# Optimization experiments

Measured on AMD Instinct MI355X. Metric: run time of the kernel, lower is better.

## Reference

```python
import jax, jax.numpy as jnp
import numpy as np

NS, NT = 4000, 4096
E_S, E_T = 64000, 65536
D_IN, D_H, N_LAYERS = 128, 256, 3
SINK_ITERS = 10
EPS = 1e-10
ALPHA = 20.0


def scatter_mean(vals, idx, n):
    # torch_geometric aggr='mean': sum then divide by count (0 where count==0)
    s = jax.ops.segment_sum(vals, idx, num_segments=n)
    c = jax.ops.segment_sum(jnp.ones((idx.shape[0],), vals.dtype), idx, num_segments=n)
    return s / jnp.maximum(c, 1.0)[:, None]


def rel_cnn(x, edge_index, layers, final_w, final_b):
    # RelCNN(batch_norm=False, cat=True, lin=True), eval mode (dropout off)
    src, dst = edge_index[0], edge_index[1]
    n = x.shape[0]
    xs = [x]
    h = x
    for (w1, w2, wr, br) in layers:
        out1 = scatter_mean((h @ w1)[src], dst, n)  # source->target mean agg
        out2 = scatter_mean((h @ w2)[dst], src, n)  # target->source mean agg
        h = jax.nn.relu(h @ wr + br + out1 + out2)  # RelConv: root + out1 + out2
        xs.append(h)
    return jnp.concatenate(xs, axis=-1) @ final_w + final_b


def sinkhorn(S):
    # Sinkhorn(max_iter=10, eps=1e-10) with dummy_row=True, exp=True, alpha=20
    ns, nt = S.shape  # ns <= nt: pad dummy rows set to eps
    pad = jnp.full((nt - ns, nt), EPS, S.dtype)
    s = jnp.concatenate([S, pad], axis=0) + EPS
    s = jnp.exp(ALPHA * s)
    for i in range(SINK_ITERS):
        if i % 2 == 1:  # row normalization
            s = s / s.sum(axis=1, keepdims=True)
        else:           # column normalization
            s = s / s.sum(axis=0, keepdims=True)
    return s[:ns, :]  # drop dummy rows


def l2norm(x):
    return x / jnp.maximum(jnp.linalg.norm(x, axis=1, keepdims=True), 1e-12)


def setup_inputs() -> dict:
    key = jax.random.key(0)
    ks = jax.random.split(key, 20)
    d = {
        'x_s': jax.random.normal(ks[0], (NS, D_IN), jnp.float32),
        'x_t': jax.random.normal(ks[1], (NT, D_IN), jnp.float32),
        'edges': jax.random.randint(ks[2], (2, E_S), 0, NS, jnp.int32),
        'edget': jax.random.randint(ks[3], (2, E_T), 0, NT, jnp.int32),
    }
    k = 4
    fan = D_IN
    for l in range(N_LAYERS):
        sc = 1.0 / np.sqrt(fan)
        d[f'W1_{l}'] = jax.random.normal(ks[k], (fan, D_H), jnp.float32) * sc; k += 1
        d[f'W2_{l}'] = jax.random.normal(ks[k], (fan, D_H), jnp.float32) * sc; k += 1
        d[f'Wr_{l}'] = jax.random.normal(ks[k], (fan, D_H), jnp.float32) * sc; k += 1
        d[f'br_{l}'] = jax.random.normal(ks[k], (D_H,), jnp.float32) * 0.01; k += 1
        fan = D_H
    fin = D_IN + N_LAYERS * D_H
    d['final_w'] = jax.random.normal(ks[k], (fin, D_H), jnp.float32) * (0.01 / np.sqrt(fin)); k += 1
    d['final_b'] = jax.random.normal(ks[k], (D_H,), jnp.float32) * 0.001
    return d


def reference(x_s, x_t, edges, edget,
              W1_0, W2_0, Wr_0, br_0,
              W1_1, W2_1, Wr_1, br_1,
              W1_2, W2_2, Wr_2, br_2,
              final_w, final_b):
    layers = [(W1_0, W2_0, Wr_0, br_0), (W1_1, W2_1, Wr_1, br_1), (W1_2, W2_2, Wr_2, br_2)]
    h_s = rel_cnn(x_s, edges, layers, final_w, final_b)   # [NS, D_H]
    h_t = rel_cnn(x_t, edget, layers, final_w, final_b)   # [NT, D_H]
    match = l2norm(h_s) @ l2norm(h_t).T                   # [NS, NT]
    return sinkhorn(match)
```

## Files before the change

### kernel.cpp

```cpp
#include <hip/hip_runtime.h>
#include <hip/hip_bf16.h>

#define NS_N 4000
#define NT_N 4096
#define NTOT 8096
#define ES_E 64000
#define ET_E 65536
#define ETOT 129536
#define D_IN 128
#define D_H 256
#define CAT_D 896
#define TMP_D 768
#define NDUM (NT_N - NS_N)
#define ALPHA_F 20.0f
#define EPS_F 1e-10f

typedef __attribute__((ext_vector_type(8))) short bf16x8;
typedef __attribute__((ext_vector_type(4))) float f32x4;

__device__ inline short f2bf(float v) {
    __hip_bfloat16 b = __float2bfloat16(v);
    return *reinterpret_cast<short*>(&b);
}
__device__ inline float bf2f(short s) {
    __hip_bfloat16 b = *reinterpret_cast<__hip_bfloat16*>(&s);
    return __bfloat162float(b);
}
__device__ inline void splitf(float v, short& hi, short& lo) {
    hi = f2bf(v);
    lo = f2bf(v - bf2f(hi));
}

typedef __attribute__((address_space(1))) const char gas_t;
typedef __attribute__((address_space(3))) char las_t;
__device__ inline void gload16(const short* g, short* l) {
    __builtin_amdgcn_global_load_lds((gas_t*)g, (las_t*)l, 16, 0, 0);
}

template<int EPI, bool COLSUM>
__global__ __launch_bounds__(256) void mfma_gemm_kernel(
    const short* __restrict__ Ahi, const short* __restrict__ Alo,
    const short* __restrict__ Bhi, const short* __restrict__ Blo,
    const float* __restrict__ bias, float* __restrict__ C,
    float* __restrict__ colacc,
    int M, int N, int K, int lda, int ldb, int ldc)
{
    __shared__ __align__(16) short sAh[2][4096];
    __shared__ __align__(16) short sAl[2][4096];
    __shared__ __align__(16) short sBh[2][4096];
    __shared__ __align__(16) short sBl[2][4096];
    const int bm = blockIdx.x * 128;
    const int bn = blockIdx.y * 128;
    const int tid = threadIdx.x;
    const int lane = tid & 63, wv = tid >> 6;
    const int wr = wv >> 1, wc = wv & 1;
    const int lr = lane & 15, lg = lane >> 4;
    const int srow = lane >> 2, sseg = (lane & 3) * 8;

    f32x4 acc[4][4];
    #pragma unroll
    for (int i = 0; i < 4; ++i)
        #pragma unroll
        for (int j = 0; j < 4; ++j) {
            f32x4 z = {0.f, 0.f, 0.f, 0.f};
            acc[i][j] = z;
        }

    auto stage = [&](int buf, int k0) {
        const short* src; short* dst; int rowbase, ld, maxrow;
        if (wv == 0)      { src = Ahi; dst = &sAh[buf][0]; rowbase = bm; ld = lda; maxrow = M - 1; }
        else if (wv == 1) { src = Alo; dst = &sAl[buf][0]; rowbase = bm; ld = lda; maxrow = M - 1; }
        else if (wv == 2) { src = Bhi; dst = &sBh[buf][0]; rowbase = bn; ld = ldb; maxrow = N - 1; }
        else              { src = Blo; dst = &sBl[buf][0]; rowbase = bn; ld = ldb; maxrow = N - 1; }
        #pragma unroll
        for (int q = 0; q < 8; ++q) {
            int gr = min(rowbase + q * 16 + srow, maxrow);
            gload16(src + (size_t)gr * ld + k0 + sseg, dst + q * 512);
        }
    };

    stage(0, 0);
    __syncthreads();
    int cur = 0;
    const int NTILES = K >> 5;
    for (int t0 = 0; t0 < NTILES; ++t0) {
        if (t0 + 1 < NTILES) stage(cur ^ 1, (t0 + 1) << 5);
        bf16x8 ah[4], al[4], bh[4], bl[4];
        #pragma unroll
        for (int i = 0; i < 4; ++i) {
            int oa = (wr * 64 + i * 16 + lr) * 32 + lg * 8;
            ah[i] = *reinterpret_cast<const bf16x8*>(&sAh[cur][oa]);
            al[i] = *reinterpret_cast<const bf16x8*>(&sAl[cur][oa]);
            int ob = (wc * 64 + i * 16 + lr) * 32 + lg * 8;
            bh[i] = *reinterpret_cast<const bf16x8*>(&sBh[cur][ob]);
            bl[i] = *reinterpret_cast<const bf16x8*>(&sBl[cur][ob]);
        }
        #pragma unroll
        for (int i = 0; i < 4; ++i)
            #pragma unroll
            for (int j = 0; j < 4; ++j) {
                acc[i][j] = __builtin_amdgcn_mfma_f32_16x16x32_bf16(ah[i], bh[j], acc[i][j], 0, 0, 0);
                acc[i][j] = __builtin_amdgcn_mfma_f32_16x16x32_bf16(ah[i], bl[j], acc[i][j], 0, 0, 0);
                acc[i][j] = __builtin_amdgcn_mfma_f32_16x16x32_bf16(al[i], bh[j], acc[i][j], 0, 0, 0);
            }
        __syncthreads();
        cur ^= 1;
    }

    float colp[4] = {0.f, 0.f, 0.f, 0.f};
    #pragma unroll
    for (int i = 0; i < 4; ++i) {
        #pragma unroll
        for (int j = 0; j < 4; ++j) {
            int col = bn + wc * 64 + j * 16 + lr;
            #pragma unroll
            for (int rr = 0; rr < 4; ++rr) {
                int row = bm + wr * 64 + i * 16 + lg * 4 + rr;
                if (row < M) {
                    float v = acc[i][j][rr];
                    if (EPI == 1) v += bias[col];
                    if (EPI == 2) v = expf(ALPHA_F * (v + EPS_F));
                    C[(size_t)row * ldc + col] = v;
                    if (COLSUM) colp[j] += v;
                }
            }
        }
    }
    if (COLSUM) {
        #pragma unroll
        for (int j = 0; j < 4; ++j) {
            float v = colp[j];
            v += __shfl_xor(v, 16);
            v += __shfl_xor(v, 32);
            if (lg == 0) atomicAdd(&colacc[bn + wc * 64 + j * 16 + lr], v);
        }
    }
}

__global__ __launch_bounds__(256) void prep_kernel(
    const float* __restrict__ xs, const float* __restrict__ xt,
    const float* __restrict__ W1a, const float* __restrict__ W2a, const float* __restrict__ Wra,
    const float* __restrict__ W1b, const float* __restrict__ W2b, const float* __restrict__ Wrb,
    const float* __restrict__ W1c, const float* __restrict__ W2c, const float* __restrict__ Wrc,
    const float* __restrict__ WF,
    short* __restrict__ WThi0, short* __restrict__ WTlo0,
    short* __restrict__ WThi1, short* __restrict__ WTlo1,
    short* __restrict__ WThi2, short* __restrict__ WTlo2,
    short* __restrict__ WFhi, short* __restrict__ WFlo,
    short* __restrict__ CAThi, short* __restrict__ CATlo,
    int* __restrict__ zbase)
{
    int blk = blockIdx.x;
    const int t = threadIdx.x;
    if (blk < 80) {
        int idx = blk * 256 + t;
        if (idx < NT_N + 2 * NTOT) zbase[idx] = 0;
        return;
    }
    blk -= 80;
    if (blk < 384 + 768 + 768) {
        const float *W1, *W2, *Wr; short *WThi, *WTlo; int K, idx;
        if (blk < 384)      { W1 = W1a; W2 = W2a; Wr = Wra; WThi = WThi0; WTlo = WTlo0; K = 128; idx = blk * 256 + t; }
        else if (blk < 1152){ W1 = W1b; W2 = W2b; Wr = Wrb; WThi = WThi1; WTlo = WTlo1; K = 256; idx = (blk - 384) * 256 + t; }
        else                { W1 = W1c; W2 = W2c; Wr = Wrc; WThi = WThi2; WTlo = WTlo2; K = 256; idx = (blk - 1152) * 256 + t; }
        int k = idx / TMP_D, c = idx % TMP_D;
        float v = (c < 256) ? W1[k * 256 + c]
                : (c < 512) ? W2[k * 256 + (c - 256)]
                            : Wr[k * 256 + (c - 512)];
        short hi, lo;
        splitf(v, hi, lo);
        WThi[(size_t)c * K + k] = hi;
        WTlo[(size_t)c * K + k] = lo;
        return;
    }
    blk -= 1920;
    if (blk < 896) {
        int idx = blk * 256 + t;
        int k = idx / D_H, n = idx % D_H;
        short hi, lo;
        splitf(WF[idx], hi, lo);
        WFhi[(size_t)n * CAT_D + k] = hi;
        WFlo[(size_t)n * CAT_D + k] = lo;
        return;
    }
    blk -= 896;
    {
        int idx = blk * 256 + t;
        int i = idx >> 7, d = idx & 127;
        float v = (i < NS_N) ? xs[(size_t)i * D_IN + d] : xt[(size_t)(i - NS_N) * D_IN + d];
        short hi, lo;
        splitf(v, hi, lo);
        CAThi[(size_t)i * CAT_D + d] = hi;
        CATlo[(size_t)i * CAT_D + d] = lo;
    }
}

__global__ void count2_kernel(const int* __restrict__ es, const int* __restrict__ et,
                              int* __restrict__ cin, int* __restrict__ cout)
{
    int e = blockIdx.x * 256 + threadIdx.x;
    int dir = blockIdx.y;
    int* cnt = dir ? cout : cin;
    if (e < ES_E) {
        int key = dir ? es[e] : es[e + ES_E];
        atomicAdd(&cnt[key], 1);
    } else if (e < ETOT) {
        int e2 = e - ES_E;
        int key = dir ? et[e2] : et[e2 + ET_E];
        atomicAdd(&cnt[key + NS_N], 1);
    }
}

__global__ __launch_bounds__(256) void scan2_kernel(const int* __restrict__ cin,
                                                    const int* __restrict__ cout,
                                                    int* __restrict__ rpin, int* __restrict__ rpout,
                                                    int* __restrict__ curin, int* __restrict__ curout)
{
    const int* cnt = blockIdx.x ? cout : cin;
    int* rowptr = blockIdx.x ? rpout : rpin;
    int* cur = blockIdx.x ? curout : curin;
    __shared__ int sums[256];
    const int t = threadIdx.x;
    const int per = (NTOT + 255) / 256;
    const int lo = t * per, hi = min((t + 1) * per, NTOT);
    int s = 0;
    for (int i = lo; i < hi; ++i) s += cnt[i];
    sums[t] = s;
    __syncthreads();
    for (int off = 1; off < 256; off <<= 1) {
        int v = (t >= off) ? sums[t - off] : 0;
        __syncthreads();
        sums[t] += v;
        __syncthreads();
    }
    int base = (t == 0) ? 0 : sums[t - 1];
    for (int i = lo; i < hi; ++i) { rowptr[i] = base; cur[i] = base; base += cnt[i]; }
    if (t == 255) rowptr[NTOT] = base;
}

__global__ void fill2_kernel(const int* __restrict__ es, const int* __restrict__ et,
                             int* __restrict__ curin, int* __restrict__ curout,
                             int* __restrict__ ciin, int* __restrict__ ciout)
{
    int e = blockIdx.x * 256 + threadIdx.x;
    int dir = blockIdx.y;
    int* cur = dir ? curout : curin;
    int* ci = dir ? ciout : ciin;
    int key, val, off;
    if (e < ES_E) {
        key = dir ? es[e] : es[e + ES_E];
        val = dir ? es[e + ES_E] : es[e];
        off = 0;
    } else if (e < ETOT) {
        int e2 = e - ES_E;
        key = dir ? et[e2] : et[e2 + ET_E];
        val = dir ? et[e2 + ET_E] : et[e2];
        off = NS_N;
    } else return;
    int pos = atomicAdd(&cur[key + off], 1);
    ci[pos] = val + off;
}

__global__ __launch_bounds__(256) void gather_combine_kernel(
    const float* __restrict__ TMP,
    const int* __restrict__ rp_in, const int* __restrict__ ci_in,
    const int* __restrict__ rp_out, const int* __restrict__ ci_out,
    const float* __restrict__ br, short* __restrict__ CAThi, short* __restrict__ CATlo,
    int catoff)
{
    int node = blockIdx.x * 4 + (threadIdx.x >> 6);
    if (node >= NTOT) return;
    int d = (threadIdx.x & 63) * 4;

    float4 a1 = make_float4(0.f, 0.f, 0.f, 0.f);
    int b0 = rp_in[node], e0 = rp_in[node + 1];
    for (int e = b0; e < e0; ++e) {
        const float4 v = *reinterpret_cast<const float4*>(&TMP[(size_t)ci_in[e] * TMP_D + d]);
        a1.x += v.x; a1.y += v.y; a1.z += v.z; a1.w += v.w;
    }
    float s1 = 1.f / (float)max(e0 - b0, 1);

    float4 a2 = make_float4(0.f, 0.f, 0.f, 0.f);
    int b1 = rp_out[node], e1 = rp_out[node + 1];
    for (int e = b1; e < e1; ++e) {
        const float4 v = *reinterpret_cast<const float4*>(&TMP[(size_t)ci_out[e] * TMP_D + 256 + d]);
        a2.x += v.x; a2.y += v.y; a2.z += v.z; a2.w += v.w;
    }
    float s2 = 1.f / (float)max(e1 - b1, 1);

    const float4 rt = *reinterpret_cast<const float4*>(&TMP[(size_t)node * TMP_D + 512 + d]);
    const float4 bb = *reinterpret_cast<const float4*>(&br[d]);
    float o[4];
    o[0] = fmaxf(rt.x + bb.x + a1.x * s1 + a2.x * s2, 0.f);
    o[1] = fmaxf(rt.y + bb.y + a1.y * s1 + a2.y * s2, 0.f);
    o[2] = fmaxf(rt.z + bb.z + a1.z * s1 + a2.z * s2, 0.f);
    o[3] = fmaxf(rt.w + bb.w + a1.w * s1 + a2.w * s2, 0.f);
    short h[4], l[4];
    #pragma unroll
    for (int q = 0; q < 4; ++q) splitf(o[q], h[q], l[q]);
    *reinterpret_cast<short4*>(&CAThi[(size_t)node * CAT_D + catoff + d]) = make_short4(h[0], h[1], h[2], h[3]);
    *reinterpret_cast<short4*>(&CATlo[(size_t)node * CAT_D + catoff + d]) = make_short4(l[0], l[1], l[2], l[3]);
}

__global__ __launch_bounds__(256) void l2norm_kernel(const float* __restrict__ in,
                                                     short* __restrict__ outhi,
                                                     short* __restrict__ outlo, int N)
{
    int row = blockIdx.x * 4 + (threadIdx.x >> 6);
    if (row >= N) return;
    int d = (threadIdx.x & 63) * 4;
    float4 v = *reinterpret_cast<const float4*>(&in[(size_t)row * D_H + d]);
    float s = v.x * v.x + v.y * v.y + v.z * v.z + v.w * v.w;
    #pragma unroll
    for (int off = 32; off; off >>= 1) s += __shfl_xor(s, off);
    float inv = 1.f / fmaxf(sqrtf(s), 1e-12f);
    float o[4] = {v.x * inv, v.y * inv, v.z * inv, v.w * inv};
    short h[4], l[4];
    #pragma unroll
    for (int q = 0; q < 4; ++q) splitf(o[q], h[q], l[q]);
    *reinterpret_cast<short4*>(&outhi[(size_t)row * D_H + d]) = make_short4(h[0], h[1], h[2], h[3]);
    *reinterpret_cast<short4*>(&outlo[(size_t)row * D_H + d]) = make_short4(l[0], l[1], l[2], l[3]);
}

__global__ __launch_bounds__(256) void colsum_kernel(
    const float* __restrict__ s0, const float* __restrict__ r, float* __restrict__ tsum)
{
    int j4 = blockIdx.x * 256 + threadIdx.x;
    int i0 = blockIdx.y * 32;
    int iend = min(i0 + 32, NS_N);
    float4 s = make_float4(0.f, 0.f, 0.f, 0.f);
    for (int i = i0; i < iend; ++i) {
        float ri = r[i];
        const float4 v = *reinterpret_cast<const float4*>(&s0[(size_t)i * NT_N + j4 * 4]);
        s.x += ri * v.x; s.y += ri * v.y; s.z += ri * v.z; s.w += ri * v.w;
    }
    atomicAdd(&tsum[j4 * 4 + 0], s.x);
    atomicAdd(&tsum[j4 * 4 + 1], s.y);
    atomicAdd(&tsum[j4 * 4 + 2], s.z);
    atomicAdd(&tsum[j4 * 4 + 3], s.w);
}

template<bool FIRST, bool FUSE_OUT>
__global__ __launch_bounds__(256) void rowsum_kernel(
    const float* __restrict__ s0, const float* __restrict__ tsum,
    const float* __restrict__ rdR, float* __restrict__ rdW,
    float* __restrict__ r, float* __restrict__ tsumNext,
    float* __restrict__ out, float dummyv)
{
    int i = blockIdx.x;
    int t = threadIdx.x;
    if (i < 16) tsumNext[i * 256 + t] = 0.f;
    float rdv = FIRST ? 1.f : rdR[0];
    float dd = (float)NDUM * dummyv * rdv;
    float s = 0.f;
    if (i < NS_N) {
        for (int j4 = t; j4 < NT_N / 4; j4 += 256) {
            const float4 v = *reinterpret_cast<const float4*>(&s0[(size_t)i * NT_N + j4 * 4]);
            const float4 ts = *reinterpret_cast<const float4*>(&tsum[j4 * 4]);
            s += v.x / (ts.x + dd) + v.y / (ts.y + dd) + v.z / (ts.z + dd) + v.w / (ts.w + dd);
        }
    } else {
        for (int j = t; j < NT_N; j += 256) s += 1.f / (tsum[j] + dd);
    }
    #pragma unroll
    for (int off = 32; off; off >>= 1) s += __shfl_xor(s, off);
    __shared__ float ws[4];
    __shared__ float ri_sh;
    if ((t & 63) == 0) ws[t >> 6] = s;
    __syncthreads();
    if (t == 0) {
        float tot = ws[0] + ws[1] + ws[2] + ws[3];
        if (i < NS_N) { r[i] = 1.f / tot; ri_sh = 1.f / tot; }
        else rdW[0] = 1.f / (dummyv * tot);
    }
    if (FUSE_OUT) {
        __syncthreads();
        if (i < NS_N) {
            float ri = ri_sh;
            for (int j4 = t; j4 < NT_N / 4; j4 += 256) {
                const float4 v = *reinterpret_cast<const float4*>(&s0[(size_t)i * NT_N + j4 * 4]);
                const float4 ts = *reinterpret_cast<const float4*>(&tsum[j4 * 4]);
                float4 o = make_float4(ri * v.x / (ts.x + dd), ri * v.y / (ts.y + dd),
                                       ri * v.z / (ts.z + dd), ri * v.w / (ts.w + dd));
                *reinterpret_cast<float4*>(&out[(size_t)i * NT_N + j4 * 4]) = o;
            }
        }
    }
}

extern "C" void kernel_launch(void* const* d_in, const int* in_sizes, int n_in,
                              void* d_out, int out_size, void* d_ws, size_t ws_size,
                              hipStream_t stream)
{
    const float* x_s = (const float*)d_in[0];
    const float* x_t = (const float*)d_in[1];
    const int* edges = (const int*)d_in[2];
    const int* edget = (const int*)d_in[3];
    const float* W1[3] = {(const float*)d_in[4], (const float*)d_in[8], (const float*)d_in[12]};
    const float* W2[3] = {(const float*)d_in[5], (const float*)d_in[9], (const float*)d_in[13]};
    const float* Wr[3] = {(const float*)d_in[6], (const float*)d_in[10], (const float*)d_in[14]};
    const float* br[3] = {(const float*)d_in[7], (const float*)d_in[11], (const float*)d_in[15]};
    const float* final_w = (const float*)d_in[16];
    const float* final_b = (const float*)d_in[17];
    float* out = (float*)d_out;

    float* W = (float*)d_ws;
    size_t off = 0;
    float* S0 = W + off;  off += (size_t)NS_N * NT_N;
    float* TMP = W + off; off += (size_t)NTOT * TMP_D;
    short* CAThi = (short*)(W + off); off += (size_t)NTOT * CAT_D / 2;
    short* CATlo = (short*)(W + off); off += (size_t)NTOT * CAT_D / 2;
    const int fan[3] = {D_IN, D_H, D_H};
    short* WThi[3]; short* WTlo[3];
    for (int l = 0; l < 3; ++l) {
        WThi[l] = (short*)(W + off); off += (size_t)TMP_D * fan[l] / 2;
        WTlo[l] = (short*)(W + off); off += (size_t)TMP_D * fan[l] / 2;
    }
    short* WFhi = (short*)(W + off); off += (size_t)D_H * CAT_D / 2;
    short* WFlo = (short*)(W + off); off += (size_t)D_H * CAT_D / 2;
    float* RVEC = W + off; off += NS_N;
    float* RD   = W + off; off += 8;
    float* TSA  = W + off; off += NT_N;
    int* CNT_IN  = (int*)(W + off); off += NTOT;
    int* CNT_OUT = (int*)(W + off); off += NTOT;
    float* TSB  = W + off; off += NT_N;
    int* RP_IN   = (int*)(W + off); off += NTOT + 1;
    int* RP_OUT  = (int*)(W + off); off += NTOT + 3;
    int* CUR_IN  = (int*)(W + off); off += NTOT;
    int* CUR_OUT = (int*)(W + off); off += NTOT;
    int* CI_IN   = (int*)(W + off); off += ETOT;
    int* CI_OUT  = (int*)(W + off); off += ETOT;
    float* HFIN = TMP;
    short* HNhi = (short*)(TMP + (size_t)NTOT * D_H);
    short* HNlo = (short*)(TMP + (size_t)NTOT * D_H + (size_t)NTOT * D_H / 2);

    const int cat_off[4] = {0, 128, 384, 640};

    prep_kernel<<<6944, 256, 0, stream>>>(
        x_s, x_t,
        W1[0], W2[0], Wr[0], W1[1], W2[1], Wr[1], W1[2], W2[2], Wr[2], final_w,
        WThi[0], WTlo[0], WThi[1], WTlo[1], WThi[2], WTlo[2], WFhi, WFlo,
        CAThi, CATlo, (int*)TSA);

    {
        dim3 gc((ETOT + 255) / 256, 2);
        count2_kernel<<<gc, 256, 0, stream>>>(edges, edget, CNT_IN, CNT_OUT);
        scan2_kernel<<<2, 256, 0, stream>>>(CNT_IN, CNT_OUT, RP_IN, RP_OUT, CUR_IN, CUR_OUT);
        fill2_kernel<<<gc, 256, 0, stream>>>(edges, edget, CUR_IN, CUR_OUT, CI_IN, CI_OUT);
    }

    for (int l = 0; l < 3; ++l) {
        dim3 gg((NTOT + 127) / 128, TMP_D / 128);
        mfma_gemm_kernel<0, false><<<gg, 256, 0, stream>>>(
            CAThi + cat_off[l], CATlo + cat_off[l], WThi[l], WTlo[l], nullptr, TMP, nullptr,
            NTOT, TMP_D, fan[l], CAT_D, fan[l], TMP_D);
        gather_combine_kernel<<<(NTOT + 3) / 4, 256, 0, stream>>>(
            TMP, RP_IN, CI_IN, RP_OUT, CI_OUT, br[l], CAThi, CATlo, cat_off[l + 1]);
    }

    {
        dim3 gf((NTOT + 127) / 128, D_H / 128);
        mfma_gemm_kernel<1, false><<<gf, 256, 0, stream>>>(
            CAThi, CATlo, WFhi, WFlo, final_b, HFIN, nullptr,
            NTOT, D_H, CAT_D, CAT_D, CAT_D, D_H);
        l2norm_kernel<<<(NTOT + 3) / 4, 256, 0, stream>>>(HFIN, HNhi, HNlo, NTOT);
    }

    {
        dim3 gm((NS_N + 127) / 128, NT_N / 128);
        mfma_gemm_kernel<2, true><<<gm, 256, 0, stream>>>(
            HNhi, HNlo, HNhi + (size_t)NS_N * D_H, HNlo + (size_t)NS_N * D_H, nullptr, S0, TSA,
            NS_N, NT_N, D_H, D_H, D_H, NT_N);
    }

    const float dummyv = expf(ALPHA_F * (EPS_F + EPS_F));
    dim3 gcs(NT_N / 1024, (NS_N + 31) / 32);
    rowsum_kernel<true, false><<<NS_N + 1, 256, 0, stream>>>(
        S0, TSA, nullptr, &RD[0], RVEC, TSB, nullptr, dummyv);
    colsum_kernel<<<gcs, 256, 0, stream>>>(S0, RVEC, TSB);
    rowsum_kernel<false, false><<<NS_N + 1, 256, 0, stream>>>(
        S0, TSB, &RD[0], &RD[1], RVEC, TSA, nullptr, dummyv);
    colsum_kernel<<<gcs, 256, 0, stream>>>(S0, RVEC, TSA);
    rowsum_kernel<false, false><<<NS_N + 1, 256, 0, stream>>>(
        S0, TSA, &RD[1], &RD[0], RVEC, TSB, nullptr, dummyv);
    colsum_kernel<<<gcs, 256, 0, stream>>>(S0, RVEC, TSB);
    rowsum_kernel<false, false><<<NS_N + 1, 256, 0, stream>>>(
        S0, TSB, &RD[0], &RD[1], RVEC, TSA, nullptr, dummyv);
    colsum_kernel<<<gcs, 256, 0, stream>>>(S0, RVEC, TSA);
    rowsum_kernel<false, true><<<NS_N + 1, 256, 0, stream>>>(
        S0, TSA, &RD[1], &RD[0], RVEC, TSB, out, dummyv);
}
```

Baseline: 580.4 us.

## Fuse Sinkhorn row/col passes, swizzle GEMM LDS, vectorize epilogue, smaller final tile

Each Sinkhorn row-normalize and column-sum pair becomes one kernel. A block of 8 rows computes the row sums against cached reciprocal column sums in LDS, then accumulates the scaled rows into the next column sums with atomics, using three rotating buffers. This halves the number of passes over the 4000x4096 S matrix. The GEMM gains an XOR-style LDS swizzle to reduce bank conflicts, swapped MFMA operands so the epilogue writes float4 rows and does float4 colsum atomics, and a BM=64 tile for the final projection to raise block count.

After: 802.7 us. 38.3% more time.

```diff
diff --git a/kernel.cpp b/kernel.cpp
--- a/kernel.cpp
+++ b/kernel.cpp
@@ -37,7 +37,7 @@
     __builtin_amdgcn_global_load_lds((gas_t*)g, (las_t*)l, 16, 0, 0);
 }
 
-template<int EPI, bool COLSUM>
+template<int BM, int EPI, bool COLSUM>
 __global__ __launch_bounds__(256) void mfma_gemm_kernel(
     const short* __restrict__ Ahi, const short* __restrict__ Alo,
     const short* __restrict__ Bhi, const short* __restrict__ Blo,
@@ -45,21 +45,22 @@
     float* __restrict__ colacc,
     int M, int N, int K, int lda, int ldb, int ldc)
 {
-    __shared__ __align__(16) short sAh[2][4096];
-    __shared__ __align__(16) short sAl[2][4096];
+    constexpr int MI = BM / 32;
+    constexpr int WH = BM / 2;
+    __shared__ __align__(16) short sAh[2][BM * 32];
+    __shared__ __align__(16) short sAl[2][BM * 32];
     __shared__ __align__(16) short sBh[2][4096];
     __shared__ __align__(16) short sBl[2][4096];
-    const int bm = blockIdx.x * 128;
+    const int bm = blockIdx.x * BM;
     const int bn = blockIdx.y * 128;
     const int tid = threadIdx.x;
     const int lane = tid & 63, wv = tid >> 6;
     const int wr = wv >> 1, wc = wv & 1;
     const int lr = lane & 15, lg = lane >> 4;
-    const int srow = lane >> 2, sseg = (lane & 3) * 8;
-
-    f32x4 acc[4][4];
+
+    f32x4 acc[MI][4];
     #pragma unroll
-    for (int i = 0; i < 4; ++i)
+    for (int i = 0; i < MI; ++i)
         #pragma unroll
         for (int j = 0; j < 4; ++j) {
             f32x4 z = {0.f, 0.f, 0.f, 0.f};
@@ -72,12 +73,17 @@
         else if (wv == 1) { src = Alo; dst = &sAl[buf][0]; rowbase = bm; ld = lda; maxrow = M - 1; }
         else if (wv == 2) { src = Bhi; dst = &sBh[buf][0]; rowbase = bn; ld = ldb; maxrow = N - 1; }
         else              { src = Blo; dst = &sBl[buf][0]; rowbase = bn; ld = ldb; maxrow = N - 1; }
+        const int nq = (wv < 2) ? (BM / 16) : 8;
         #pragma unroll
         for (int q = 0; q < 8; ++q) {
-            int gr = min(rowbase + q * 16 + srow, maxrow);
-            gload16(src + (size_t)gr * ld + k0 + sseg, dst + q * 512);
+            if (q >= nq) break;
+            int row = q * 16 + (lane >> 2);
+            int seg = ((lane & 3) - (row >> 1)) & 3;
+            int gr = min(rowbase + row, maxrow);
+            gload16(src + (size_t)gr * ld + k0 + seg * 8, dst + (q * 64 + lane) * 8);
         }
     };
+    auto ldsoff = [](int row, int g) { return (row * 4 + ((g + (row >> 1)) & 3)) * 8; };
 
     stage(0, 0);
     __syncthreads();
@@ -85,43 +91,57 @@
     const int NTILES = K >> 5;
     for (int t0 = 0; t0 < NTILES; ++t0) {
         if (t0 + 1 < NTILES) stage(cur ^ 1, (t0 + 1) << 5);
-        bf16x8 ah[4], al[4], bh[4], bl[4];
-        #pragma unroll
-        for (int i = 0; i < 4; ++i) {
-            int oa = (wr * 64 + i * 16 + lr) * 32 + lg * 8;
+        bf16x8 ah[MI], al[MI], bh[4], bl[4];
+        #pragma unroll
+        for (int i = 0; i < MI; ++i) {
+            int oa = ldsoff(wr * WH + i * 16 + lr, lg);
             ah[i] = *reinterpret_cast<const bf16x8*>(&sAh[cur][oa]);
             al[i] = *reinterpret_cast<const bf16x8*>(&sAl[cur][oa]);
-            int ob = (wc * 64 + i * 16 + lr) * 32 + lg * 8;
-            bh[i] = *reinterpret_cast<const bf16x8*>(&sBh[cur][ob]);
-            bl[i] = *reinterpret_cast<const bf16x8*>(&sBl[cur][ob]);
-        }
-        #pragma unroll
-        for (int i = 0; i < 4; ++i)
+        }
+        #pragma unroll
+        for (int j = 0; j < 4; ++j) {
+            int ob = ldsoff(wc * 64 + j * 16 + lr, lg);
+            bh[j] = *reinterpret_cast<const bf16x8*>(&sBh[cur][ob]);
+            bl[j] = *reinterpret_cast<const bf16x8*>(&sBl[cur][ob]);
+        }
+        #pragma unroll
+        for (int i = 0; i < MI; ++i)
             #pragma unroll
             for (int j = 0; j < 4; ++j) {
-                acc[i][j] = __builtin_amdgcn_mfma_f32_16x16x32_bf16(ah[i], bh[j], acc[i][j], 0, 0, 0);
-                acc[i][j] = __builtin_amdgcn_mfma_f32_16x16x32_bf16(ah[i], bl[j], acc[i][j], 0, 0, 0);
-                acc[i][j] = __builtin_amdgcn_mfma_f32_16x16x32_bf16(al[i], bh[j], acc[i][j], 0, 0, 0);
+                acc[i][j] = __builtin_amdgcn_mfma_f32_16x16x32_bf16(bh[j], ah[i], acc[i][j], 0, 0, 0);
+                acc[i][j] = __builtin_amdgcn_mfma_f32_16x16x32_bf16(bl[j], ah[i], acc[i][j], 0, 0, 0);
+                acc[i][j] = __builtin_amdgcn_mfma_f32_16x16x32_bf16(bh[j], al[i], acc[i][j], 0, 0, 0);
             }
         __syncthreads();
         cur ^= 1;
     }
 
-    float colp[4] = {0.f, 0.f, 0.f, 0.f};
+    float4 csum[4];
+    if (COLSUM) {
+        #pragma unroll
+        for (int j = 0; j < 4; ++j) csum[j] = make_float4(0.f, 0.f, 0.f, 0.f);
+    }
     #pragma unroll
-    for (int i = 0; i < 4; ++i) {
-        #pragma unroll
-        for (int j = 0; j < 4; ++j) {
-            int col = bn + wc * 64 + j * 16 + lr;
+    for (int i = 0; i < MI; ++i) {
+        int row = bm + wr * WH + i * 16 + lr;
+        if (row < M) {
             #pragma unroll
-            for (int rr = 0; rr < 4; ++rr) {
-                int row = bm + wr * 64 + i * 16 + lg * 4 + rr;
-                if (row < M) {
-                    float v = acc[i][j][rr];
-                    if (EPI == 1) v += bias[col];
-                    if (EPI == 2) v = expf(ALPHA_F * (v + EPS_F));
-                    C[(size_t)row * ldc + col] = v;
-                    if (COLSUM) colp[j] += v;
+            for (int j = 0; j < 4; ++j) {
+                int col = bn + wc * 64 + j * 16 + lg * 4;
+                float4 v = make_float4(acc[i][j][0], acc[i][j][1], acc[i][j][2], acc[i][j][3]);
+                if (EPI == 1) {
+                    const float4 bb = *reinterpret_cast<const float4*>(&bias[col]);
+                    v.x += bb.x; v.y += bb.y; v.z += bb.z; v.w += bb.w;
+                }
+                if (EPI == 2) {
+                    v.x = expf(ALPHA_F * (v.x + EPS_F));
+                    v.y = expf(ALPHA_F * (v.y + EPS_F));
+                    v.z = expf(ALPHA_F * (v.z + EPS_F));
+                    v.w = expf(ALPHA_F * (v.w + EPS_F));
+                }
+                *reinterpret_cast<float4*>(&C[(size_t)row * ldc + col]) = v;
+                if (COLSUM) {
+                    csum[j].x += v.x; csum[j].y += v.y; csum[j].z += v.z; csum[j].w += v.w;
                 }
             }
         }
@@ -129,14 +149,24 @@
     if (COLSUM) {
         #pragma unroll
         for (int j = 0; j < 4; ++j) {
-            float v = colp[j];
-            v += __shfl_xor(v, 16);
-            v += __shfl_xor(v, 32);
-            if (lg == 0) atomicAdd(&colacc[bn + wc * 64 + j * 16 + lr], v);
-        }
-    }
-}
-
+            float4 t = csum[j];
+            #pragma unroll
+            for (int m = 1; m < 16; m <<= 1) {
+                t.x += __shfl_xor(t.x, m); t.y += __shfl_xor(t.y, m);
+                t.z += __shfl_xor(t.z, m); t.w += __shfl_xor(t.w, m);
+            }
+            if (lr == 0) {
+                int col = bn + wc * 64 + j * 16 + lg * 4;
+                atomicAdd(&colacc[col + 0], t.x);
+                atomicAdd(&colacc[col + 1], t.y);
+                atomicAdd(&colacc[col + 2], t.z);
+                atomicAdd(&colacc[col + 3], t.w);
+            }
+        }
+    }
+}
+
+#define ZERO_N (NT_N + 2 * NTOT + NT_N)
 __global__ __launch_bounds__(256) void prep_kernel(
     const float* __restrict__ xs, const float* __restrict__ xt,
     const float* __restrict__ W1a, const float* __restrict__ W2a, const float* __restrict__ Wra,
@@ -152,12 +182,12 @@
 {
     int blk = blockIdx.x;
     const int t = threadIdx.x;
-    if (blk < 80) {
+    if (blk < 96) {
         int idx = blk * 256 + t;
-        if (idx < NT_N + 2 * NTOT) zbase[idx] = 0;
+        if (idx < ZERO_N) zbase[idx] = 0;
         return;
     }
-    blk -= 80;
+    blk -= 96;
     if (blk < 384 + 768 + 768) {
         const float *W1, *W2, *Wr; short *WThi, *WTlo; int K, idx;
         if (blk < 384)      { W1 = W1a; W2 = W2a; Wr = Wra; WThi = WThi0; WTlo = WTlo0; K = 128; idx = blk * 256 + t; }
@@ -322,68 +352,95 @@
     *reinterpret_cast<short4*>(&outlo[(size_t)row * D_H + d]) = make_short4(l[0], l[1], l[2], l[3]);
 }
 
-__global__ __launch_bounds__(256) void colsum_kernel(
-    const float* __restrict__ s0, const float* __restrict__ r, float* __restrict__ tsum)
-{
-    int j4 = blockIdx.x * 256 + threadIdx.x;
-    int i0 = blockIdx.y * 32;
-    int iend = min(i0 + 32, NS_N);
-    float4 s = make_float4(0.f, 0.f, 0.f, 0.f);
-    for (int i = i0; i < iend; ++i) {
-        float ri = r[i];
-        const float4 v = *reinterpret_cast<const float4*>(&s0[(size_t)i * NT_N + j4 * 4]);
-        s.x += ri * v.x; s.y += ri * v.y; s.z += ri * v.z; s.w += ri * v.w;
-    }
-    atomicAdd(&tsum[j4 * 4 + 0], s.x);
-    atomicAdd(&tsum[j4 * 4 + 1], s.y);
-    atomicAdd(&tsum[j4 * 4 + 2], s.z);
-    atomicAdd(&tsum[j4 * 4 + 3], s.w);
-}
-
-template<bool FIRST, bool FUSE_OUT>
-__global__ __launch_bounds__(256) void rowsum_kernel(
+template<bool FIRST, bool OUT>
+__global__ __launch_bounds__(256) void sinkfuse_kernel(
     const float* __restrict__ s0, const float* __restrict__ tsum,
     const float* __restrict__ rdR, float* __restrict__ rdW,
-    float* __restrict__ r, float* __restrict__ tsumNext,
+    float* __restrict__ tsnext, float* __restrict__ tszero,
     float* __restrict__ out, float dummyv)
 {
-    int i = blockIdx.x;
-    int t = threadIdx.x;
-    if (i < 16) tsumNext[i * 256 + t] = 0.f;
-    float rdv = FIRST ? 1.f : rdR[0];
-    float dd = (float)NDUM * dummyv * rdv;
-    float s = 0.f;
-    if (i < NS_N) {
-        for (int j4 = t; j4 < NT_N / 4; j4 += 256) {
-            const float4 v = *reinterpret_cast<const float4*>(&s0[(size_t)i * NT_N + j4 * 4]);
-            const float4 ts = *reinterpret_cast<const float4*>(&tsum[j4 * 4]);
-            s += v.x / (ts.x + dd) + v.y / (ts.y + dd) + v.z / (ts.z + dd) + v.w / (ts.w + dd);
-        }
-    } else {
-        for (int j = t; j < NT_N; j += 256) s += 1.f / (tsum[j] + dd);
-    }
+    const int bid = blockIdx.x;
+    const int t = threadIdx.x;
+    if (!OUT && bid >= 501) {
+        tszero[(bid - 501) * 256 + t] = 0.f;
+        return;
+    }
+    __shared__ float4 cl[1024];
+    __shared__ float wsred[4];
+    const float dd = (float)NDUM * dummyv * (FIRST ? 1.f : rdR[0]);
+    const float4* ts4 = reinterpret_cast<const float4*>(tsum);
     #pragma unroll
-    for (int off = 32; off; off >>= 1) s += __shfl_xor(s, off);
-    __shared__ float ws[4];
-    __shared__ float ri_sh;
-    if ((t & 63) == 0) ws[t >> 6] = s;
+    for (int k = 0; k < 4; ++k) {
+        int j4 = t + k * 256;
+        float4 ts = ts4[j4];
+        cl[j4] = make_float4(1.f / (ts.x + dd), 1.f / (ts.y + dd),
+                             1.f / (ts.z + dd), 1.f / (ts.w + dd));
+    }
     __syncthreads();
-    if (t == 0) {
-        float tot = ws[0] + ws[1] + ws[2] + ws[3];
-        if (i < NS_N) { r[i] = 1.f / tot; ri_sh = 1.f / tot; }
-        else rdW[0] = 1.f / (dummyv * tot);
-    }
-    if (FUSE_OUT) {
+
+    if (bid >= 500) {
+        float s = 0.f;
+        #pragma unroll
+        for (int k = 0; k < 4; ++k) {
+            float4 c = cl[t + k * 256];
+            s += c.x + c.y + c.z + c.w;
+        }
+        #pragma unroll
+        for (int m = 1; m < 64; m <<= 1) s += __shfl_xor(s, m);
+        if ((t & 63) == 0) wsred[t >> 6] = s;
         __syncthreads();
-        if (i < NS_N) {
-            float ri = ri_sh;
-            for (int j4 = t; j4 < NT_N / 4; j4 += 256) {
-                const float4 v = *reinterpret_cast<const float4*>(&s0[(size_t)i * NT_N + j4 * 4]);
-                const float4 ts = *reinterpret_cast<const float4*>(&tsum[j4 * 4]);
-                float4 o = make_float4(ri * v.x / (ts.x + dd), ri * v.y / (ts.y + dd),
-                                       ri * v.z / (ts.z + dd), ri * v.w / (ts.w + dd));
-                *reinterpret_cast<float4*>(&out[(size_t)i * NT_N + j4 * 4]) = o;
+        if (t == 0) rdW[0] = 1.f / (dummyv * (wsred[0] + wsred[1] + wsred[2] + wsred[3]));
+        return;
+    }
+
+    float4 cacc[4];
+    if (!OUT) {
+        #pragma unroll
+        for (int k = 0; k < 4; ++k) cacc[k] = make_float4(0.f, 0.f, 0.f, 0.f);
+    }
+    for (int r8 = 0; r8 < 8; ++r8) {
+        int row = bid * 8 + r8;
+        const float4* rowp = reinterpret_cast<const float4*>(s0 + (size_t)row * NT_N);
+        float4 v[4];
+        float s = 0.f;
+        #pragma unroll
+        for (int k = 0; k < 4; ++k) {
+            int j4 = t + k * 256;
+            v[k] = rowp[j4];
+            float4 c = cl[j4];
+            s += v[k].x * c.x + v[k].y * c.y + v[k].z * c.z + v[k].w * c.w;
+        }
+        #pragma unroll
+        for (int m = 1; m < 64; m <<= 1) s += __shfl_xor(s, m);
+        if ((t & 63) == 0) wsred[t >> 6] = s;
+        __syncthreads();
+        float ri = 1.f / (wsred[0] + wsred[1] + wsred[2] + wsred[3]);
+        __syncthreads();
+        if (OUT) {
+            float4* outp = reinterpret_cast<float4*>(out + (size_t)row * NT_N);
+            #pragma unroll
+            for (int k = 0; k < 4; ++k) {
+                int j4 = t + k * 256;
+                float4 c = cl[j4];
+                outp[j4] = make_float4(ri * v[k].x * c.x, ri * v[k].y * c.y,
+                                       ri * v[k].z * c.z, ri * v[k].w * c.w);
             }
+        } else {
+            #pragma unroll
+            for (int k = 0; k < 4; ++k) {
+                cacc[k].x += ri * v[k].x; cacc[k].y += ri * v[k].y;
+                cacc[k].z += ri * v[k].z; cacc[k].w += ri * v[k].w;
+            }
+        }
+    }
+    if (!OUT) {
+        #pragma unroll
+        for (int k = 0; k < 4; ++k) {
+            int j = (t + k * 256) * 4;
+            atomicAdd(&tsnext[j + 0], cacc[k].x);
+            atomicAdd(&tsnext[j + 1], cacc[k].y);
+            atomicAdd(&tsnext[j + 2], cacc[k].z);
+            atomicAdd(&tsnext[j + 3], cacc[k].w);
         }
     }
 }
@@ -418,12 +475,12 @@
     }
     short* WFhi = (short*)(W + off); off += (size_t)D_H * CAT_D / 2;
     short* WFlo = (short*)(W + off); off += (size_t)D_H * CAT_D / 2;
-    float* RVEC = W + off; off += NS_N;
     float* RD   = W + off; off += 8;
     float* TSA  = W + off; off += NT_N;
     int* CNT_IN  = (int*)(W + off); off += NTOT;
     int* CNT_OUT = (int*)(W + off); off += NTOT;
     float* TSB  = W + off; off += NT_N;
+    float* TSC  = W + off; off += NT_N;
     int* RP_IN   = (int*)(W + off); off += NTOT + 1;
     int* RP_OUT  = (int*)(W + off); off += NTOT + 3;
     int* CUR_IN  = (int*)(W + off); off += NTOT;
@@ -436,7 +493,7 @@
 
     const int cat_off[4] = {0, 128, 384, 640};
 
-    prep_kernel<<<6944, 256, 0, stream>>>(
+    prep_kernel<<<6960, 256, 0, stream>>>(
         x_s, x_t,
         W1[0], W2[0], Wr[0], W1[1], W2[1], Wr[1], W1[2], W2[2], Wr[2], final_w,
         WThi[0], WTlo[0], WThi[1], WTlo[1], WThi[2], WTlo[2], WFhi, WFlo,
@@ -451,7 +508,7 @@
 
     for (int l = 0; l < 3; ++l) {
         dim3 gg((NTOT + 127) / 128, TMP_D / 128);
-        mfma_gemm_kernel<0, false><<<gg, 256, 0, stream>>>(
+        mfma_gemm_kernel<128, 0, false><<<gg, 256, 0, stream>>>(
             CAThi + cat_off[l], CATlo + cat_off[l], WThi[l], WTlo[l], nullptr, TMP, nullptr,
             NTOT, TMP_D, fan[l], CAT_D, fan[l], TMP_D);
         gather_combine_kernel<<<(NTOT + 3) / 4, 256, 0, stream>>>(
@@ -459,8 +516,8 @@
     }
 
     {
-        dim3 gf((NTOT + 127) / 128, D_H / 128);
-        mfma_gemm_kernel<1, false><<<gf, 256, 0, stream>>>(
+        dim3 gf((NTOT + 63) / 64, D_H / 128);
+        mfma_gemm_kernel<64, 1, false><<<gf, 256, 0, stream>>>(
             CAThi, CATlo, WFhi, WFlo, final_b, HFIN, nullptr,
             NTOT, D_H, CAT_D, CAT_D, CAT_D, D_H);
         l2norm_kernel<<<(NTOT + 3) / 4, 256, 0, stream>>>(HFIN, HNhi, HNlo, NTOT);
@@ -468,25 +525,20 @@
 
     {
         dim3 gm((NS_N + 127) / 128, NT_N / 128);
-        mfma_gemm_kernel<2, true><<<gm, 256, 0, stream>>>(
+        mfma_gemm_kernel<128, 2, true><<<gm, 256, 0, stream>>>(
             HNhi, HNlo, HNhi + (size_t)NS_N * D_H, HNlo + (size_t)NS_N * D_H, nullptr, S0, TSA,
             NS_N, NT_N, D_H, D_H, D_H, NT_N);
     }
 
     const float dummyv = expf(ALPHA_F * (EPS_F + EPS_F));
-    dim3 gcs(NT_N / 1024, (NS_N + 31) / 32);
-    rowsum_kernel<true, false><<<NS_N + 1, 256, 0, stream>>>(
-        S0, TSA, nullptr, &RD[0], RVEC, TSB, nullptr, dummyv);
-    colsum_kernel<<<gcs, 256, 0, stream>>>(S0, RVEC, TSB);
-    rowsum_kernel<false, false><<<NS_N + 1, 256, 0, stream>>>(
-        S0, TSB, &RD[0], &RD[1], RVEC, TSA, nullptr, dummyv);
-    colsum_kernel<<<gcs, 256, 0, stream>>>(S0, RVEC, TSA);
-    rowsum_kernel<false, false><<<NS_N + 1, 256, 0, stream>>>(
-        S0, TSA, &RD[1], &RD[0], RVEC, TSB, nullptr, dummyv);
-    colsum_kernel<<<gcs, 256, 0, stream>>>(S0, RVEC, TSB);
-    rowsum_kernel<false, false><<<NS_N + 1, 256, 0, stream>>>(
-        S0, TSB, &RD[0], &RD[1], RVEC, TSA, nullptr, dummyv);
-    colsum_kernel<<<gcs, 256, 0, stream>>>(S0, RVEC, TSA);
-    rowsum_kernel<false, true><<<NS_N + 1, 256, 0, stream>>>(
-        S0, TSA, &RD[1], &RD[0], RVEC, TSB, out, dummyv);
-}
+    sinkfuse_kernel<true, false><<<517, 256, 0, stream>>>(
+        S0, TSA, nullptr, &RD[0], TSB, TSC, nullptr, dummyv);
+    sinkfuse_kernel<false, false><<<517, 256, 0, stream>>>(
+        S0, TSB, &RD[0], &RD[1], TSC, TSA, nullptr, dummyv);
+    sinkfuse_kernel<false, false><<<517, 256, 0, stream>>>(
+        S0, TSC, &RD[1], &RD[0], TSA, TSB, nullptr, dummyv);
+    sinkfuse_kernel<false, false><<<517, 256, 0, stream>>>(
+        S0, TSA, &RD[0], &RD[1], TSB, TSC, nullptr, dummyv);
+    sinkfuse_kernel<false, true><<<500, 256, 0, stream>>>(
+        S0, TSB, &RD[1], nullptr, nullptr, nullptr, out, dummyv);
+}
```
